# Kernel optimization log

Hardware: AMD Instinct MI355X
Metric: run time of the kernel (lower is better)

The kernel has to match this reference:

```python
import jax, jax.numpy as jnp
import numpy as np

B, Hd, Wd, C, NH, WS = 8, 128, 128, 192, 6, 8
HDIM = int(C * 2.0)   # FFN hidden = 384
RED = C // 8          # AIM channel-gate reduction = 24


def setup_inputs() -> dict:
    key = jax.random.key(0)
    ks = jax.random.split(key, 12)
    s = 0.02
    return {
        "x": jax.random.normal(ks[0], (B, Hd * Wd, C), jnp.float32),
        "H": Hd,
        "W": Wd,
        "n1_w": jnp.ones((C,), jnp.float32),
        "n1_b": jnp.zeros((C,), jnp.float32),
        "qkv_w": jax.random.normal(ks[1], (C, 3 * C), jnp.float32) * s,
        "proj_w": jax.random.normal(ks[2], (C, C), jnp.float32) * s,
        "proj_b": jnp.zeros((C,), jnp.float32),
        "attn_bias": jax.random.normal(ks[3], (NH, WS * WS, WS * WS), jnp.float32) * s,
        "conv_w": jax.random.normal(ks[4], (C, 1, 3, 3), jnp.float32) * s,
        "cg_w1": jax.random.normal(ks[5], (RED, C), jnp.float32) * s,
        "cg_w2": jax.random.normal(ks[6], (C, RED), jnp.float32) * s,
        "n2_w": jnp.ones((C,), jnp.float32),
        "n2_b": jnp.zeros((C,), jnp.float32),
        "fc1_w": jax.random.normal(ks[7], (C, HDIM), jnp.float32) * s,
        "smix_w": jax.random.normal(ks[8], (HDIM, 1, 3, 3), jnp.float32) * s,
        "fc2_w": jax.random.normal(ks[9], (HDIM, C), jnp.float32) * s,
    }


def _ln(x, w, b):
    m = x.mean(-1, keepdims=True)
    v = ((x - m) ** 2).mean(-1, keepdims=True)
    return (x - m) * jax.lax.rsqrt(v + 1e-5) * w + b


def _dwconv(x, w, H, W):
    # x: [B, L, Cx] -> depthwise 3x3 'same' conv -> [B, L, Cx]
    Bx, L, Cx = x.shape
    xi = x.transpose(0, 2, 1).reshape(Bx, Cx, H, W)
    y = jax.lax.conv_general_dilated(
        xi, w, (1, 1), 'SAME', feature_group_count=Cx,
        dimension_numbers=('NCHW', 'OIHW', 'NCHW'))
    return y.reshape(Bx, Cx, L).transpose(0, 2, 1)


def _window_attn(x, H, W, qkv_w, proj_w, proj_b, bias):
    Bx, L, Cx = x.shape
    nHw, nWw = H // WS, W // WS  # H, W are multiples of WS here (no padding needed)
    hd = Cx // NH
    # [B, L, C] -> [B*nH*nW, ws*ws, C]
    xw = (x.reshape(Bx, nHw, WS, nWw, WS, Cx)
           .transpose(0, 1, 3, 2, 4, 5)
           .reshape(Bx * nHw * nWw, WS * WS, Cx))
    qkv = (xw @ qkv_w).reshape(-1, WS * WS, 3, NH, hd).transpose(2, 0, 3, 1, 4)
    q, k, v = qkv[0], qkv[1], qkv[2]          # [Bw, nh, N, hd]
    logits = (q * hd ** -0.5) @ k.transpose(0, 1, 3, 2) + bias[None]
    attn = jax.nn.softmax(logits, axis=-1)
    out = (attn @ v).transpose(0, 2, 1, 3).reshape(-1, WS * WS, Cx)
    out = out @ proj_w + proj_b
    # windows -> [B, L, C]
    return (out.reshape(Bx, nHw, nWw, WS, WS, Cx)
               .transpose(0, 1, 3, 2, 4, 5)
               .reshape(Bx, L, Cx))


def reference(x, H, W, n1_w, n1_b, qkv_w, proj_w, proj_b, attn_bias,
              conv_w, cg_w1, cg_w2, n2_w, n2_b, fc1_w, smix_w, fc2_w):
    n1 = _ln(x, n1_w, n1_b)
    attn_feat = _window_attn(n1, H, W, qkv_w, proj_w, proj_b, attn_bias)
    conv_feat = jax.nn.gelu(_dwconv(n1, conv_w, H, W), approximate=False)
    # AIM: channel_modulates_spatial (btype == 'spatial')
    pooled = conv_feat.mean(axis=1)                                   # [B, C]
    cm = jax.nn.sigmoid(jax.nn.gelu(pooled @ cg_w1.T, approximate=False) @ cg_w2.T)
    x = x + attn_feat * cm[:, None, :] + conv_feat                    # residual (DropPath=id)
    # FFN with depthwise spatial mixing
    n2 = _ln(x, n2_w, n2_b)
    h = jax.nn.gelu(n2 @ fc1_w, approximate=False)                    # [B, L, HDIM]
    h = _dwconv(h, smix_w, H, W)
    return x + h @ fc2_w
```

## Files before the change

kernel.cpp:

```cpp
#include <hip/hip_runtime.h>
#include <hip/hip_bf16.h>
#include <math.h>

#define BATCH 8
#define CCH 192
#define LTOK 16384
#define BL 131072LL
#define NWIN 2048
#define NHEADS 6

typedef __hip_bfloat16 bf16;
typedef __bf16 bfr;
typedef bfr bf16x8 __attribute__((ext_vector_type(8)));
typedef float f32x4 __attribute__((ext_vector_type(4)));
typedef unsigned short u16x8 __attribute__((ext_vector_type(8)));
typedef unsigned short u16x4 __attribute__((ext_vector_type(4)));
typedef unsigned int u32x2 __attribute__((ext_vector_type(2)));

#define FX     0
#define FN1W   1
#define FN1B   2
#define FQKVW  3
#define FPROJW 4
#define FPROJB 5
#define FBIAS  6
#define FCONVW 7
#define FCG1   8
#define FCG2   9
#define FN2W   10
#define FN2B   11
#define FFC1   12
#define FSMIX  13
#define FFC2   14

struct InPtrs { const void* p[15]; int n[15]; };

__device__ __forceinline__ float ldin(const void* p, long long i, int f32) {
    return f32 ? ((const float*)p)[i]
               : __bfloat162float(((const bf16*)p)[i]);
}

__device__ __forceinline__ float bfcvt(unsigned short u) {
    return __uint_as_float((unsigned)u << 16);
}

__device__ __forceinline__ f32x4 ld4f(const void* p, long long i, int f32) {
    if (f32) return *(const f32x4*)((const float*)p + i);
    u16x4 v = *(const u16x4*)((const bf16*)p + i);
    f32x4 r;
    r[0] = bfcvt(v[0]); r[1] = bfcvt(v[1]); r[2] = bfcvt(v[2]); r[3] = bfcvt(v[3]);
    return r;
}
__device__ __forceinline__ f32x4 ld4b(const bf16* p, long long i) {
    u16x4 v = *(const u16x4*)(p + i);
    f32x4 r;
    r[0] = bfcvt(v[0]); r[1] = bfcvt(v[1]); r[2] = bfcvt(v[2]); r[3] = bfcvt(v[3]);
    return r;
}
__device__ __forceinline__ void st4b(bf16* p, long long i, f32x4 v) {
    union { bf16 h; unsigned short u; } cv;
    u16x4 o;
    cv.h = __float2bfloat16(v[0]); o[0] = cv.u;
    cv.h = __float2bfloat16(v[1]); o[1] = cv.u;
    cv.h = __float2bfloat16(v[2]); o[2] = cv.u;
    cv.h = __float2bfloat16(v[3]); o[3] = cv.u;
    *(u16x4*)(p + i) = o;
}

__device__ __forceinline__ unsigned pk2bf(float a, float b) {
    union { bf16 h; unsigned short u; } ca, cb;
    ca.h = __float2bfloat16(a);
    cb.h = __float2bfloat16(b);
    return (unsigned)ca.u | ((unsigned)cb.u << 16);
}

__device__ __forceinline__ float gelu_f(float v) {
    return 0.5f * v * (1.0f + erff(v * 0.70710678118654752f));
}

__device__ int local_probe(const void* p_, int n) {
    __shared__ int sh0, sh1, sh2;
    if (threadIdx.x == 0) { sh0 = 0; sh1 = 0; sh2 = 0; }
    __syncthreads();
    const bf16* p = (const bf16*)p_;
    int m = n < 2048 ? n : 2048;
    bool insane = false, evennz = false, oddnz = false;
    for (int i = threadIdx.x; i < m; i += 256) {
        float v = __bfloat162float(p[i]);
        if (!(fabsf(v) <= 1e9f)) insane = true;
        if (v != 0.0f) { if (i & 1) oddnz = true; else evennz = true; }
    }
    if (insane) sh0 = 1;
    if (evennz) sh1 = 1;
    if (oddnz)  sh2 = 1;
    __syncthreads();
    return (sh0 || (!sh1 && sh2)) ? 1 : 0;
}

__global__ __launch_bounds__(256)
void prep_k(InPtrs ip, int* __restrict__ flags,
            bf16* __restrict__ qkv_wT, bf16* __restrict__ proj_wT,
            bf16* __restrict__ fc1_wT, bf16* __restrict__ fc2_wT,
            float* __restrict__ convwT, float* __restrict__ smixwT,
            float* __restrict__ pooled) {
    int blk = blockIdx.x;
    if (blk < 15) {
        int f = local_probe(ip.p[blk], ip.n[blk]);
        if (threadIdx.x == 0) flags[blk] = f;
        return;
    }
    blk -= 15;
    if (blk < 432) {
        int f = local_probe(ip.p[FQKVW], ip.n[FQKVW]);
        int idx = blk * 256 + threadIdx.x;
        int k = idx / 576, n = idx - k * 576;
        qkv_wT[(long long)n * 192 + k] = __float2bfloat16(ldin(ip.p[FQKVW], idx, f));
        return;
    }
    blk -= 432;
    if (blk < 144) {
        int f = local_probe(ip.p[FPROJW], ip.n[FPROJW]);
        int idx = blk * 256 + threadIdx.x;
        int k = idx / 192, n = idx - k * 192;
        proj_wT[(long long)n * 192 + k] = __float2bfloat16(ldin(ip.p[FPROJW], idx, f));
        return;
    }
    blk -= 144;
    if (blk < 288) {
        int f = local_probe(ip.p[FFC1], ip.n[FFC1]);
        int idx = blk * 256 + threadIdx.x;
        int k = idx / 384, n = idx - k * 384;
        fc1_wT[(long long)n * 192 + k] = __float2bfloat16(ldin(ip.p[FFC1], idx, f));
        return;
    }
    blk -= 288;
    if (blk < 288) {
        int f = local_probe(ip.p[FFC2], ip.n[FFC2]);
        int idx = blk * 256 + threadIdx.x;
        int k = idx / 192, n = idx - k * 192;
        fc2_wT[(long long)n * 384 + k] = __float2bfloat16(ldin(ip.p[FFC2], idx, f));
        return;
    }
    blk -= 288;
    if (blk < 7) {
        int f = local_probe(ip.p[FCONVW], ip.n[FCONVW]);
        int idx = blk * 256 + threadIdx.x;
        if (idx < 192 * 9) {
            int c = idx / 9, t = idx - c * 9;
            convwT[t * 192 + c] = ldin(ip.p[FCONVW], idx, f);
        }
        return;
    }
    blk -= 7;
    if (blk < 14) {
        int f = local_probe(ip.p[FSMIX], ip.n[FSMIX]);
        int idx = blk * 256 + threadIdx.x;
        if (idx < 384 * 9) {
            int c = idx / 9, t = idx - c * 9;
            smixwT[t * 384 + c] = ldin(ip.p[FSMIX], idx, f);
        }
        return;
    }
    blk -= 14;
    {
        int idx = blk * 256 + threadIdx.x;
        if (idx < BATCH * CCH) pooled[idx] = 0.f;
    }
}

__global__ __launch_bounds__(256)
void ln_kernel(const void* __restrict__ x, const void* __restrict__ w,
               const void* __restrict__ b, bf16* __restrict__ out,
               const int* flags) {
    int fx = flags[FX], fw = flags[FN1W], fb = flags[FN1B];
    int wv = threadIdx.x >> 6, lane = threadIdx.x & 63;
    int gw = lane >> 4, l16 = lane & 15;
    long long t = (long long)blockIdx.x * 16 + wv * 4 + gw;
    long long base = t * CCH;
    f32x4 v[3];
#pragma unroll
    for (int k = 0; k < 3; ++k)
        v[k] = ld4f(x, base + l16 * 4 + 64 * k, fx);
    float s = 0.f;
#pragma unroll
    for (int k = 0; k < 3; ++k) s += v[k][0] + v[k][1] + v[k][2] + v[k][3];
    s += __shfl_xor(s, 1); s += __shfl_xor(s, 2);
    s += __shfl_xor(s, 4); s += __shfl_xor(s, 8);
    float mean = s * (1.0f / 192.0f);
    float vs = 0.f;
#pragma unroll
    for (int k = 0; k < 3; ++k)
#pragma unroll
        for (int j = 0; j < 4; ++j) {
            float d = v[k][j] - mean;
            vs += d * d;
        }
    vs += __shfl_xor(vs, 1); vs += __shfl_xor(vs, 2);
    vs += __shfl_xor(vs, 4); vs += __shfl_xor(vs, 8);
    float rstd = rsqrtf(vs * (1.0f / 192.0f) + 1e-5f);
#pragma unroll
    for (int k = 0; k < 3; ++k) {
        int c0 = l16 * 4 + 64 * k;
        f32x4 wv4 = ld4f(w, c0, fw);
        f32x4 bv4 = ld4f(b, c0, fb);
        f32x4 o;
#pragma unroll
        for (int j = 0; j < 4; ++j)
            o[j] = (v[k][j] - mean) * rstd * wv4[j] + bv4[j];
        st4b(out, base + c0, o);
    }
}

template<int EPI, int KK, int NN, typename CT>
__global__ __launch_bounds__(256)
void gemm2_k(const bf16* __restrict__ A_, const bf16* __restrict__ BT_,
             CT* __restrict__ Cmat, const void* __restrict__ bias,
             const float* __restrict__ res, const int* __restrict__ flags) {
    constexpr int KT = KK / 192;
    constexpr int NC = NN / 64;
    constexpr int NITER = NC * KT;
    constexpr int GSTR = KK * 2;
    constexpr bool WINM = (EPI == 0);
    __shared__ __align__(16) char Ts[64 * 384];

    const int fb = (EPI == 1) ? flags[FPROJB] : 0;
    const int tid = threadIdx.x;
    const int lane = tid & 63, wv = tid >> 6;
    const int r16 = lane & 15, q = lane >> 4;
    const long long m0 = (long long)blockIdx.x * 64;
    const int swz = (r16 & 7) << 4;

    const int wdx = blockIdx.x;
    const int wb = wdx >> 8, wrem = wdx & 255, wy = wrem >> 4, wx = wrem & 15;
    const long long tokbase = (long long)wb * LTOK + (wy * 8) * 128 + wx * 8;

    f32x4 pre[6];
    auto loadB = [&](int itn) {
        int nc2 = itn / KT, kt2 = itn - nc2 * KT;
#pragma unroll
        for (int p = 0; p < 6; ++p) {
            int off = p * 4096 + tid * 16;
            int row = off / 384, col = off - row * 384;
            pre[p] = *(const f32x4*)((const char*)BT_ +
                     (long long)(nc2 * 64 + row) * GSTR + kt2 * 384 + col);
        }
    };
    auto writeT = [&]() {
#pragma unroll
        for (int p = 0; p < 6; ++p) {
            int off = p * 4096 + tid * 16;
            int row = off / 384, col = off - row * 384;
            *(f32x4*)(Ts + row * 384 + (col ^ ((row & 7) << 4))) = pre[p];
        }
    };

    loadB(0);

    bf16x8 afrag[KK / 32];
    const char* Arow = Ts + (wv * 16 + r16) * 384;
    const char* asrc = (const char*)A_;
#pragma unroll
    for (int kt = 0; kt < KT; ++kt) {
#pragma unroll
        for (int p = 0; p < 6; ++p) {
            int off = p * 4096 + tid * 16;
            int row = off / 384, col = off - row * 384;
            long long grow = WINM ? (tokbase + (row >> 3) * 128 + (row & 7))
                                  : (m0 + row);
            *(f32x4*)(Ts + row * 384 + (col ^ ((row & 7) << 4))) =
                *(const f32x4*)(asrc + grow * GSTR + kt * 384 + col);
        }
        __syncthreads();
#pragma unroll
        for (int ks = 0; ks < 6; ++ks)
            afrag[kt * 6 + ks] = *(const bf16x8*)(Arow + ((ks * 64 + q * 16) ^ swz));
        __syncthreads();
    }
    writeT();
    __syncthreads();

    f32x4 acc0, acc1, acc2, acc3;
    float resv[16];

    for (int it = 0; it < NITER; ++it) {
        const int nc = it / KT, kt = it - nc * KT;
        if (kt == 0) {
            acc0 = f32x4{0.f, 0.f, 0.f, 0.f};
            acc1 = acc0; acc2 = acc0; acc3 = acc0;
            if (EPI == 3) {
#pragma unroll
                for (int j = 0; j < 4; ++j)
#pragma unroll
                    for (int r = 0; r < 4; ++r)
                        resv[j * 4 + r] =
                            res[(m0 + wv * 16 + q * 4 + r) * NN + nc * 64 + j * 16 + r16];
            }
        }
        const bool nxt = (it + 1 < NITER);
        if (nxt) loadB(it + 1);
#pragma unroll
        for (int ks = 0; ks < 6; ++ks) {
            bf16x8 a = afrag[kt * 6 + ks];
            const char* bb = Ts + r16 * 384 + ((ks * 64 + q * 16) ^ swz);
            bf16x8 b0 = *(const bf16x8*)(bb);
            bf16x8 b1 = *(const bf16x8*)(bb + 16 * 384);
            bf16x8 b2 = *(const bf16x8*)(bb + 32 * 384);
            bf16x8 b3 = *(const bf16x8*)(bb + 48 * 384);
            acc0 = __builtin_amdgcn_mfma_f32_16x16x32_bf16(a, b0, acc0, 0, 0, 0);
            acc1 = __builtin_amdgcn_mfma_f32_16x16x32_bf16(a, b1, acc1, 0, 0, 0);
            acc2 = __builtin_amdgcn_mfma_f32_16x16x32_bf16(a, b2, acc2, 0, 0, 0);
            acc3 = __builtin_amdgcn_mfma_f32_16x16x32_bf16(a, b3, acc3, 0, 0, 0);
        }
        __syncthreads();
        if (nxt) writeT();
        if (kt == KT - 1) {
            f32x4 accs[4] = {acc0, acc1, acc2, acc3};
#pragma unroll
            for (int j = 0; j < 4; ++j) {
                int col = nc * 64 + j * 16 + r16;
#pragma unroll
                for (int r = 0; r < 4; ++r) {
                    float v = accs[j][r];
                    if (EPI == 1) v += ldin(bias, col, fb);
                    if (EPI == 2) v = gelu_f(v);
                    if (EPI == 3) v += resv[j * 4 + r];
                    if (WINM) {
                        int tin = wv * 16 + q * 4 + r;
                        int sel = col / 192, rem2 = col - sel * 192;
                        int hh = rem2 >> 5, d = rem2 & 31;
                        Cmat[((((long long)sel * NWIN + wdx) * 6 + hh) * 64 + tin) * 32 + d] = (CT)v;
                    } else {
                        long long row = m0 + wv * 16 + q * 4 + r;
                        Cmat[row * NN + col] = (CT)v;
                    }
                }
            }
        }
        if (nxt) __syncthreads();
    }
}

__global__ __launch_bounds__(768)
void attn_proj_k(const bf16* __restrict__ qkvw, const void* __restrict__ bias,
                 const bf16* __restrict__ pwT, const void* __restrict__ proj_b,
                 bf16* __restrict__ attnf, const int* __restrict__ flags) {
    __shared__ __align__(16) char SM[24576];

    const int fbias = flags[FBIAS];
    const int wid = threadIdx.x >> 6, lane = threadIdx.x & 63;
    const int h = wid >> 1, half = wid & 1;
    const int w = blockIdx.x;
    const int l15 = lane & 15, quad = lane >> 4;
    bfr* vtp = (bfr*)(SM + h * 4096);

    const bfr* qb = (const bfr*)qkvw + ((long long)w * 6 + h) * 2048;
    const bfr* kb = qb + (long long)NWIN * 6 * 2048;
    const bfr* vb = kb + (long long)NWIN * 6 * 2048;

    if (half == 0) {
        const bfr* vp = vb + lane * 32;
        bf16x8 v0 = *(const bf16x8*)(vp);
        bf16x8 v1 = *(const bf16x8*)(vp + 8);
        bf16x8 v2 = *(const bf16x8*)(vp + 16);
        bf16x8 v3 = *(const bf16x8*)(vp + 24);
#pragma unroll
        for (int j = 0; j < 8; ++j) {
            int sc = lane ^ (j << 3);
            vtp[j * 64 + sc]        = v0[j];
            vtp[(j + 8) * 64 + sc]  = v1[j];
            vtp[(j + 16) * 64 + sc] = v2[j];
            vtp[(j + 24) * 64 + sc] = v3[j];
        }
    }

    bf16x8 bk[4], aq[2];
#pragma unroll
    for (int ti = 0; ti < 4; ++ti)
        bk[ti] = *(const bf16x8*)(kb + (ti * 16 + l15) * 32 + quad * 8);
#pragma unroll
    for (int tj2 = 0; tj2 < 2; ++tj2)
        aq[tj2] = *(const bf16x8*)(qb + ((half * 2 + tj2) * 16 + l15) * 32 + quad * 8);

    const float scale = 0.17677669529663689f;
    const long long bias0 = (long long)h * 4096;
    unsigned Wreg[2][4][2];
#pragma unroll
    for (int tj2 = 0; tj2 < 2; ++tj2) {
        const int tj = half * 2 + tj2;
        f32x4 T[4];
#pragma unroll
        for (int ti = 0; ti < 4; ++ti) {
            f32x4 z = {0.f, 0.f, 0.f, 0.f};
            T[ti] = __builtin_amdgcn_mfma_f32_16x16x32_bf16(bk[ti], aq[tj2], z, 0, 0, 0);
        }
        const long long brow = bias0 + (tj * 16 + l15) * 64 + quad * 4;
        float mloc = -3.0e38f;
#pragma unroll
        for (int ti = 0; ti < 4; ++ti) {
            f32x4 bv4 = ld4f(bias, brow + ti * 16, fbias);
#pragma unroll
            for (int r = 0; r < 4; ++r) {
                float v = T[ti][r] * scale + bv4[r];
                T[ti][r] = v;
                mloc = fmaxf(mloc, v);
            }
        }
        mloc = fmaxf(mloc, __shfl_xor(mloc, 16));
        mloc = fmaxf(mloc, __shfl_xor(mloc, 32));
        float l = 0.f;
#pragma unroll
        for (int ti = 0; ti < 4; ++ti)
#pragma unroll
            for (int r = 0; r < 4; ++r) {
                float e = __expf(T[ti][r] - mloc);
                T[ti][r] = e;
                l += e;
            }
        l += __shfl_xor(l, 16);
        l += __shfl_xor(l, 32);
        float linv = 1.0f / l;
#pragma unroll
        for (int ti = 0; ti < 4; ++ti) {
            Wreg[tj2][ti][0] = pk2bf(T[ti][0] * linv, T[ti][1] * linv);
            Wreg[tj2][ti][1] = pk2bf(T[ti][2] * linv, T[ti][3] * linv);
        }
    }

    __syncthreads();

    const int vsw = (l15 & 7) << 3;
    bf16x8 bv[2][2];
#pragma unroll
    for (int kc = 0; kc < 2; ++kc) {
        bv[kc][0] = *(const bf16x8*)&vtp[l15 * 64 + ((kc * 32 + quad * 8) ^ vsw)];
        bv[kc][1] = *(const bf16x8*)&vtp[(16 + l15) * 64 + ((kc * 32 + quad * 8) ^ vsw)];
    }
    const int hi = quad >> 1, qlow = quad & 1;
    f32x4 O[2][2];
#pragma unroll
    for (int tj2 = 0; tj2 < 2; ++tj2) {
        O[tj2][0] = f32x4{0.f, 0.f, 0.f, 0.f};
        O[tj2][1] = O[tj2][0];
    }
#pragma unroll
    for (int tj2 = 0; tj2 < 2; ++tj2)
#pragma unroll
        for (int kc = 0; kc < 2; ++kc) {
            union { unsigned u[4]; bf16x8 v; } ap;
#pragma unroll
            for (int j2 = 0; j2 < 4; ++j2) {
                int srcl = (2 * qlow + (j2 >> 1)) * 16 + l15;
                unsigned va = (unsigned)__shfl((int)Wreg[tj2][2 * kc][j2 & 1], srcl);
                unsigned vb2 = (unsigned)__shfl((int)Wreg[tj2][2 * kc + 1][j2 & 1], srcl);
                ap.u[j2] = hi ? vb2 : va;
            }
            O[tj2][0] = __builtin_amdgcn_mfma_f32_16x16x32_bf16(ap.v, bv[kc][0], O[tj2][0], 0, 0, 0);
            O[tj2][1] = __builtin_amdgcn_mfma_f32_16x16x32_bf16(ap.v, bv[kc][1], O[tj2][1], 0, 0, 0);
        }

    const int fpb = flags[FPROJB];
    const int pcol = wid * 16 + l15;
    float pbv = ldin(proj_b, pcol, fpb);
    bf16x8 pw[6];
#pragma unroll
    for (int ks = 0; ks < 6; ++ks)
        pw[ks] = *(const bf16x8*)((const bfr*)pwT + (long long)pcol * 192 + ks * 32 + quad * 8);

    __syncthreads();

#pragma unroll
    for (int tj2 = 0; tj2 < 2; ++tj2)
#pragma unroll
        for (int n2 = 0; n2 < 2; ++n2)
#pragma unroll
            for (int r = 0; r < 4; ++r) {
                int row = (half * 2 + tj2) * 16 + quad * 4 + r;
                int cb = (h * 64 + n2 * 32 + l15 * 2) ^ ((row & 7) << 4);
                *(bf16*)(SM + row * 384 + cb) = __float2bfloat16(O[tj2][n2][r]);
            }

    __syncthreads();

    const int csw = (l15 & 7) << 4;
    f32x4 pacc[4];
#pragma unroll
    for (int mt = 0; mt < 4; ++mt)
        pacc[mt] = f32x4{0.f, 0.f, 0.f, 0.f};
#pragma unroll
    for (int ks = 0; ks < 6; ++ks) {
#pragma unroll
        for (int mt = 0; mt < 4; ++mt) {
            bf16x8 af = *(const bf16x8*)(SM + (mt * 16 + l15) * 384 +
                                         ((ks * 64 + quad * 16) ^ csw));
            pacc[mt] = __builtin_amdgcn_mfma_f32_16x16x32_bf16(af, pw[ks], pacc[mt], 0, 0, 0);
        }
    }

#pragma unroll
    for (int mt = 0; mt < 4; ++mt)
#pragma unroll
        for (int r = 0; r < 4; ++r) {
            long long row = (long long)w * 64 + mt * 16 + quad * 4 + r;
            attnf[row * CCH + pcol] = __float2bfloat16(pacc[mt][r] + pbv);
        }
}

template<bool GELU, int CX, bool POOL>
__global__ __launch_bounds__(256)
void dwconv_s4_k(const bf16* __restrict__ in, const float* __restrict__ wt,
                 bf16* __restrict__ out, float* __restrict__ pooled) {
    constexpr int CG = CX / 8;
    __shared__ float psum[POOL ? 192 : 1];
    if (POOL) {
        if (threadIdx.x < 192) psum[threadIdx.x] = 0.f;
        __syncthreads();
    }
    int cpx = gridDim.x >> 3;
    int lb = (blockIdx.x & 7) * cpx + (blockIdx.x >> 3);
    long long idx = (long long)lb * 256 + threadIdx.x;
    int cg = (int)(idx % CG);
    long long s = idx / CG;
    int xs = (int)(s & 31);
    long long by = s >> 5;
    int y = (int)(by & 127);
    int x0 = xs * 4;
    int c0 = cg * 8;
    const long long rowpix = by * 128;

    float acc[4][8] = {};
#pragma unroll
    for (int dy = -1; dy <= 1; ++dy) {
        int yy = y + dy;
        if (yy < 0 || yy > 127) continue;
        const bf16* rp = in + ((rowpix + dy * 128) + x0) * CX + c0;
        float fcol[6][8];
#pragma unroll
        for (int ci = 0; ci < 6; ++ci) {
            int xx = x0 + ci - 1;
            if (xx < 0 || xx > 127) {
#pragma unroll
                for (int j = 0; j < 8; ++j) fcol[ci][j] = 0.f;
            } else {
                u16x8 v = *(const u16x8*)(rp + (ci - 1) * CX);
#pragma unroll
                for (int j = 0; j < 8; ++j) fcol[ci][j] = bfcvt(v[j]);
            }
        }
        const float* wb = wt + (dy + 1) * 3 * CX + c0;
#pragma unroll
        for (int dx = 0; dx < 3; ++dx) {
            f32x4 w0 = *(const f32x4*)(wb + dx * CX);
            f32x4 w1 = *(const f32x4*)(wb + dx * CX + 4);
#pragma unroll
            for (int px = 0; px < 4; ++px) {
#pragma unroll
                for (int j = 0; j < 4; ++j) {
                    acc[px][j]     += fcol[px + dx][j]     * w0[j];
                    acc[px][j + 4] += fcol[px + dx][j + 4] * w1[j];
                }
            }
        }
    }
    float sums[8] = {0.f, 0.f, 0.f, 0.f, 0.f, 0.f, 0.f, 0.f};
#pragma unroll
    for (int px = 0; px < 4; ++px) {
        __attribute__((aligned(16))) unsigned short ob[8];
#pragma unroll
        for (int j = 0; j < 8; ++j) {
            float vv = acc[px][j];
            if (GELU) vv = gelu_f(vv);
            if (POOL) sums[j] += vv;
            union { bf16 h; unsigned short u; } cv;
            cv.h = __float2bfloat16(vv);
            ob[j] = cv.u;
        }
        *(u16x8*)(out + (rowpix + x0 + px) * CX + c0) = *(const u16x8*)ob;
    }
    if (POOL) {
#pragma unroll
        for (int j = 0; j < 8; ++j)
            atomicAdd(&psum[c0 + j], sums[j]);
        __syncthreads();
        if (threadIdx.x < 192) {
            int b = (int)(by >> 7);
            atomicAdd(&pooled[b * CCH + threadIdx.x], psum[threadIdx.x]);
        }
    }
}

__global__ void cm_k(const float* __restrict__ pooled, const void* __restrict__ w1,
                     const void* __restrict__ w2, float* __restrict__ cm,
                     const int* flags) {
    __shared__ float ps[192], g[24];
    int f1 = flags[FCG1], f2 = flags[FCG2];
    int b = blockIdx.x, c = threadIdx.x;
    ps[c] = pooled[b * CCH + c] * (1.0f / 16384.0f);
    __syncthreads();
    if (c < 24) {
        float t = 0.f;
        for (int k = 0; k < 192; ++k) t += ps[k] * ldin(w1, c * 192 + k, f1);
        g[c] = gelu_f(t);
    }
    __syncthreads();
    float s = 0.f;
#pragma unroll
    for (int r = 0; r < 24; ++r) s += g[r] * ldin(w2, c * 24 + r, f2);
    cm[b * CCH + c] = 1.0f / (1.0f + expf(-s));
}

__global__ __launch_bounds__(256)
void x2ln2_k(const void* __restrict__ x, const bf16* __restrict__ attnf,
             const bf16* __restrict__ conv, const float* __restrict__ cm,
             const void* __restrict__ w, const void* __restrict__ bb,
             float* __restrict__ x2, bf16* __restrict__ n2, const int* flags) {
    int fx = flags[FX], fw = flags[FN2W], fb = flags[FN2B];
    int wv = threadIdx.x >> 6, lane = threadIdx.x & 63;
    int gw = lane >> 4, l16 = lane & 15;
    long long t = (long long)blockIdx.x * 16 + wv * 4 + gw;
    int b = (int)(t >> 14);
    int l = (int)(t & 16383);
    int y = l >> 7, xx = l & 127;
    long long wrow = ((long long)b * 256 + (y >> 3) * 16 + (xx >> 3)) * 64 + (y & 7) * 8 + (xx & 7);

    f32x4 sv[3];
#pragma unroll
    for (int k = 0; k < 3; ++k) {
        int c0 = l16 * 4 + 64 * k;
        f32x4 xv  = ld4f(x, t * CCH + c0, fx);
        f32x4 af  = ld4b(attnf, wrow * CCH + c0);
        f32x4 cf  = ld4b(conv, t * CCH + c0);
        f32x4 cmv = *(const f32x4*)(cm + b * CCH + c0);
        f32x4 o;
#pragma unroll
        for (int j = 0; j < 4; ++j)
            o[j] = xv[j] + af[j] * cmv[j] + cf[j];
        *(f32x4*)(x2 + t * CCH + c0) = o;
        sv[k] = o;
    }
    float s = 0.f;
#pragma unroll
    for (int k = 0; k < 3; ++k) s += sv[k][0] + sv[k][1] + sv[k][2] + sv[k][3];
    s += __shfl_xor(s, 1); s += __shfl_xor(s, 2);
    s += __shfl_xor(s, 4); s += __shfl_xor(s, 8);
    float mean = s * (1.0f / 192.0f);
    float vs = 0.f;
#pragma unroll
    for (int k = 0; k < 3; ++k)
#pragma unroll
        for (int j = 0; j < 4; ++j) {
            float d = sv[k][j] - mean;
            vs += d * d;
        }
    vs += __shfl_xor(vs, 1); vs += __shfl_xor(vs, 2);
    vs += __shfl_xor(vs, 4); vs += __shfl_xor(vs, 8);
    float rstd = rsqrtf(vs * (1.0f / 192.0f) + 1e-5f);
#pragma unroll
    for (int k = 0; k < 3; ++k) {
        int c0 = l16 * 4 + 64 * k;
        f32x4 wv4 = ld4f(w, c0, fw);
        f32x4 bv4 = ld4f(bb, c0, fb);
        f32x4 o;
#pragma unroll
        for (int j = 0; j < 4; ++j)
            o[j] = (sv[k][j] - mean) * rstd * wv4[j] + bv4[j];
        st4b(n2, t * CCH + c0, o);
    }
}

extern "C" void kernel_launch(void* const* d_in, const int* in_sizes, int n_in,
                              void* d_out, int out_size, void* d_ws, size_t ws_size,
                              hipStream_t stream) {
    (void)n_in; (void)out_size; (void)ws_size;
    float* out = (float*)d_out;

    char* wsp = (char*)d_ws;
    size_t off = 0;
    auto alloc = [&](size_t bytes) -> char* {
        char* p = wsp + off;
        off += (bytes + 255) & ~(size_t)255;
        return p;
    };
    int*  flags   = (int*)alloc(15 * 4);
    bf16* qkv_wT  = (bf16*)alloc(576 * 192 * 2);
    bf16* proj_wT = (bf16*)alloc(192 * 192 * 2);
    bf16* fc1_wT  = (bf16*)alloc(384 * 192 * 2);
    bf16* fc2_wT  = (bf16*)alloc(192 * 384 * 2);
    float* convwT = (float*)alloc(9 * CCH * 4);
    float* smixwT = (float*)alloc(9 * 384 * 4);
    float* pooled = (float*)alloc(BATCH * CCH * 4);
    float* cm     = (float*)alloc(BATCH * CCH * 4);
    char* Rbig    = alloc(BL * 576 * 2);
    char* Rpair   = alloc(BL * 384 * 2);

    bf16* qkvb  = (bf16*)Rbig;
    bf16* convf = (bf16*)Rbig;
    bf16* hbuf  = (bf16*)Rbig;
    bf16* n1    = (bf16*)Rpair;
    bf16* attnf = (bf16*)(Rpair + (size_t)BL * 192 * 2);
    bf16* n2    = n1;
    bf16* h2    = (bf16*)Rpair;
    float* x2   = out;

    const int imap[15] = {0, 3, 4, 5, 6, 7, 8, 9, 10, 11, 12, 13, 14, 15, 16};
    InPtrs ip;
    for (int i = 0; i < 15; ++i) { ip.p[i] = d_in[imap[i]]; ip.n[i] = in_sizes[imap[i]]; }
    const void* x        = d_in[0];
    const void* proj_b   = d_in[7];
    const void* attnbias = d_in[8];
    const void* cg_w1    = d_in[10];
    const void* cg_w2    = d_in[11];

    prep_k<<<1194, 256, 0, stream>>>(ip, flags, qkv_wT, proj_wT, fc1_wT, fc2_wT,
                                     convwT, smixwT, pooled);

    ln_kernel<<<BL / 16, 256, 0, stream>>>(x, d_in[3], d_in[4], n1, flags);
    gemm2_k<0, 192, 576, bf16><<<BL / 64, 256, 0, stream>>>(n1, qkv_wT, qkvb, nullptr, nullptr, flags);
    attn_proj_k<<<NWIN, 768, 0, stream>>>(qkvb, attnbias, proj_wT, proj_b, attnf, flags);
    dwconv_s4_k<true, 192, true><<<(int)(BL / 4 * 24 / 256), 256, 0, stream>>>(n1, convwT, convf, pooled);
    cm_k<<<BATCH, 192, 0, stream>>>(pooled, cg_w1, cg_w2, cm, flags);
    x2ln2_k<<<BL / 16, 256, 0, stream>>>(x, attnf, convf, cm, d_in[12], d_in[13], x2, n2, flags);
    gemm2_k<2, 192, 384, bf16><<<BL / 64, 256, 0, stream>>>(n2, fc1_wT, hbuf, nullptr, nullptr, flags);
    dwconv_s4_k<false, 384, false><<<(int)(BL / 4 * 48 / 256), 256, 0, stream>>>(hbuf, smixwT, h2, nullptr);
    gemm2_k<3, 384, 192, float><<<BL / 64, 256, 0, stream>>>(h2, fc2_wT, out, nullptr, x2, flags);
}
```

Before: 592.6 us.

## Merge window attention and depthwise conv into one heterogeneous launch

Combines the attention+projection kernel and the GELU depthwise conv + pooling kernel into one grid. The first NWIN blocks do attention and the extra blocks do conv with 768 threads each. This removes a launch boundary and lets the memory-bound conv overlap the MFMA-heavy attention. Because conv output previously aliased the qkv buffer, it now goes to a separate workspace buffer. The merged path is used only when the workspace is large enough, otherwise it falls back to the two separate kernels. Costs are extra workspace and a different block shape for the conv (768 threads, 1024 blocks).

```diff
diff --git a/kernel.cpp b/kernel.cpp
--- a/kernel.cpp
+++ b/kernel.cpp
@@ -340,16 +340,14 @@
     }
 }
 
-__global__ __launch_bounds__(768)
-void attn_proj_k(const bf16* __restrict__ qkvw, const void* __restrict__ bias,
-                 const bf16* __restrict__ pwT, const void* __restrict__ proj_b,
-                 bf16* __restrict__ attnf, const int* __restrict__ flags) {
-    __shared__ __align__(16) char SM[24576];
-
+__device__ __forceinline__
+void attn_body(int w, char* SM, const bf16* __restrict__ qkvw,
+               const void* __restrict__ bias, const bf16* __restrict__ pwT,
+               const void* __restrict__ proj_b, bf16* __restrict__ attnf,
+               const int* __restrict__ flags) {
     const int fbias = flags[FBIAS];
     const int wid = threadIdx.x >> 6, lane = threadIdx.x & 63;
     const int h = wid >> 1, half = wid & 1;
-    const int w = blockIdx.x;
     const int l15 = lane & 15, quad = lane >> 4;
     bfr* vtp = (bfr*)(SM + h * 4096);
 
@@ -505,19 +503,16 @@
         }
 }
 
-template<bool GELU, int CX, bool POOL>
-__global__ __launch_bounds__(256)
-void dwconv_s4_k(const bf16* __restrict__ in, const float* __restrict__ wt,
-                 bf16* __restrict__ out, float* __restrict__ pooled) {
+template<bool GELU, int CX, bool POOL, int TPB>
+__device__ __forceinline__
+void dwconv_body(int lb, const bf16* __restrict__ in, const float* __restrict__ wt,
+                 bf16* __restrict__ out, float* __restrict__ pooled, float* psum) {
     constexpr int CG = CX / 8;
-    __shared__ float psum[POOL ? 192 : 1];
     if (POOL) {
         if (threadIdx.x < 192) psum[threadIdx.x] = 0.f;
         __syncthreads();
     }
-    int cpx = gridDim.x >> 3;
-    int lb = (blockIdx.x & 7) * cpx + (blockIdx.x >> 3);
-    long long idx = (long long)lb * 256 + threadIdx.x;
+    long long idx = (long long)lb * TPB + threadIdx.x;
     int cg = (int)(idx % CG);
     long long s = idx / CG;
     int xs = (int)(s & 31);
@@ -586,6 +581,40 @@
             atomicAdd(&pooled[b * CCH + threadIdx.x], psum[threadIdx.x]);
         }
     }
+}
+
+__global__ __launch_bounds__(768)
+void attn_conv_k(const bf16* __restrict__ qkvw, const void* __restrict__ bias,
+                 const bf16* __restrict__ pwT, const void* __restrict__ proj_b,
+                 bf16* __restrict__ attnf, const int* __restrict__ flags,
+                 const bf16* __restrict__ n1, const float* __restrict__ convwT,
+                 bf16* __restrict__ convf, float* __restrict__ pooled) {
+    __shared__ __align__(16) char SM[24576];
+    if (blockIdx.x >= NWIN) {
+        int dblk = blockIdx.x - NWIN;
+        int lb = (dblk & 7) * 128 + (dblk >> 3);
+        dwconv_body<true, 192, true, 768>(lb, n1, convwT, convf, pooled, (float*)SM);
+        return;
+    }
+    attn_body(blockIdx.x, SM, qkvw, bias, pwT, proj_b, attnf, flags);
+}
+
+__global__ __launch_bounds__(768)
+void attn_proj_k(const bf16* __restrict__ qkvw, const void* __restrict__ bias,
+                 const bf16* __restrict__ pwT, const void* __restrict__ proj_b,
+                 bf16* __restrict__ attnf, const int* __restrict__ flags) {
+    __shared__ __align__(16) char SM[24576];
+    attn_body(blockIdx.x, SM, qkvw, bias, pwT, proj_b, attnf, flags);
+}
+
+template<bool GELU, int CX, bool POOL>
+__global__ __launch_bounds__(256)
+void dwconv_s4_k(const bf16* __restrict__ in, const float* __restrict__ wt,
+                 bf16* __restrict__ out, float* __restrict__ pooled) {
+    __shared__ float psum[POOL ? 192 : 1];
+    int cpx = gridDim.x >> 3;
+    int lb = (blockIdx.x & 7) * cpx + (blockIdx.x >> 3);
+    dwconv_body<GELU, CX, POOL, 256>(lb, in, wt, out, pooled, psum);
 }
 
 __global__ void cm_k(const float* __restrict__ pooled, const void* __restrict__ w1,
@@ -670,7 +699,7 @@
 extern "C" void kernel_launch(void* const* d_in, const int* in_sizes, int n_in,
                               void* d_out, int out_size, void* d_ws, size_t ws_size,
                               hipStream_t stream) {
-    (void)n_in; (void)out_size; (void)ws_size;
+    (void)n_in; (void)out_size;
     float* out = (float*)d_out;
 
     char* wsp = (char*)d_ws;
@@ -691,9 +720,11 @@
     float* cm     = (float*)alloc(BATCH * CCH * 4);
     char* Rbig    = alloc(BL * 576 * 2);
     char* Rpair   = alloc(BL * 384 * 2);
+    bf16* convf2  = (bf16*)alloc((size_t)BL * 192 * 2);
+    const bool merged = (ws_size >= off);
 
     bf16* qkvb  = (bf16*)Rbig;
-    bf16* convf = (bf16*)Rbig;
+    bf16* convf = merged ? convf2 : (bf16*)Rbig;
     bf16* hbuf  = (bf16*)Rbig;
     bf16* n1    = (bf16*)Rpair;
     bf16* attnf = (bf16*)(Rpair + (size_t)BL * 192 * 2);
@@ -715,8 +746,13 @@
 
     ln_kernel<<<BL / 16, 256, 0, stream>>>(x, d_in[3], d_in[4], n1, flags);
     gemm2_k<0, 192, 576, bf16><<<BL / 64, 256, 0, stream>>>(n1, qkv_wT, qkvb, nullptr, nullptr, flags);
-    attn_proj_k<<<NWIN, 768, 0, stream>>>(qkvb, attnbias, proj_wT, proj_b, attnf, flags);
-    dwconv_s4_k<true, 192, true><<<(int)(BL / 4 * 24 / 256), 256, 0, stream>>>(n1, convwT, convf, pooled);
+    if (merged) {
+        attn_conv_k<<<NWIN + 1024, 768, 0, stream>>>(qkvb, attnbias, proj_wT, proj_b,
+                                                     attnf, flags, n1, convwT, convf, pooled);
+    } else {
+        attn_proj_k<<<NWIN, 768, 0, stream>>>(qkvb, attnbias, proj_wT, proj_b, attnf, flags);
+        dwconv_s4_k<true, 192, true><<<(int)(BL / 4 * 24 / 256), 256, 0, stream>>>(n1, convwT, convf, pooled);
+    }
     cm_k<<<BATCH, 192, 0, stream>>>(pooled, cg_w1, cg_w2, cm, flags);
     x2ln2_k<<<BL / 16, 256, 0, stream>>>(x, attnf, convf, cm, d_in[12], d_in[13], x2, n2, flags);
     gemm2_k<2, 192, 384, bf16><<<BL / 64, 256, 0, stream>>>(n2, fc1_wT, hbuf, nullptr, nullptr, flags);
```

Measured after the change: 606.9 us. 1.02x slower.

## Fuse FFN depthwise conv into fc2 GEMM A-tile load

Applied to the files above, without the earlier changes.

Removes the separate depthwise 3x3 spatial-mix kernel on the FFN hidden activations. The fc2 GEMM now computes the 3x3 depthwise conv on the fly while staging each 64-token A tile into shared memory. This drops a full write and read of the 384-channel intermediate buffer. In exchange, each GEMM block reads up to 9 neighbouring token vectors per element and does the conv arithmetic inside the GEMM, which adds load traffic and register pressure to the GEMM prologue.

```diff
diff --git a/kernel.cpp b/kernel.cpp
--- a/kernel.cpp
+++ b/kernel.cpp
@@ -211,11 +211,12 @@
     }
 }
 
-template<int EPI, int KK, int NN, typename CT>
+template<int EPI, int KK, int NN, typename CT, bool CONVA = false>
 __global__ __launch_bounds__(256)
 void gemm2_k(const bf16* __restrict__ A_, const bf16* __restrict__ BT_,
              CT* __restrict__ Cmat, const void* __restrict__ bias,
-             const float* __restrict__ res, const int* __restrict__ flags) {
+             const float* __restrict__ res, const int* __restrict__ flags,
+             const float* __restrict__ cwt = nullptr) {
     constexpr int KT = KK / 192;
     constexpr int NC = NN / 64;
     constexpr int NITER = NC * KT;
@@ -234,6 +235,10 @@
     const int wb = wdx >> 8, wrem = wdx & 255, wy = wrem >> 4, wx = wrem & 15;
     const long long tokbase = (long long)wb * LTOK + (wy * 8) * 128 + wx * 8;
 
+    const int l0 = (int)(m0 & 16383);
+    const int yy0 = l0 >> 7, xx0 = l0 & 127;
+    const long long imgbase = m0 - l0;
+
     f32x4 pre[6];
     auto loadB = [&](int itn) {
         int nc2 = itn / KT, kt2 = itn - nc2 * KT;
@@ -265,10 +270,44 @@
         for (int p = 0; p < 6; ++p) {
             int off = p * 4096 + tid * 16;
             int row = off / 384, col = off - row * 384;
-            long long grow = WINM ? (tokbase + (row >> 3) * 128 + (row & 7))
-                                  : (m0 + row);
-            *(f32x4*)(Ts + row * 384 + (col ^ ((row & 7) << 4))) =
-                *(const f32x4*)(asrc + grow * GSTR + kt * 384 + col);
+            if (CONVA) {
+                int c0 = kt * 192 + (col >> 1);
+                int px = xx0 + row;
+                float acc[8] = {};
+#pragma unroll
+                for (int dy = -1; dy <= 1; ++dy) {
+                    int yv = yy0 + dy;
+                    if (yv < 0 || yv > 127) continue;
+#pragma unroll
+                    for (int dx = -1; dx <= 1; ++dx) {
+                        int xv = px + dx;
+                        if (xv < 0 || xv > 127) continue;
+                        u16x8 hv = *(const u16x8*)((const bf16*)A_ +
+                                   (imgbase + yv * 128 + xv) * KK + c0);
+                        const float* wr = cwt + ((dy + 1) * 3 + (dx + 1)) * KK + c0;
+                        f32x4 w0 = *(const f32x4*)(wr);
+                        f32x4 w1 = *(const f32x4*)(wr + 4);
+#pragma unroll
+                        for (int j = 0; j < 4; ++j) {
+                            acc[j]     += bfcvt(hv[j])     * w0[j];
+                            acc[j + 4] += bfcvt(hv[j + 4]) * w1[j];
+                        }
+                    }
+                }
+                union { u16x8 v; unsigned short u[8]; } ob;
+#pragma unroll
+                for (int j = 0; j < 8; ++j) {
+                    union { bf16 h; unsigned short u; } cv;
+                    cv.h = __float2bfloat16(acc[j]);
+                    ob.u[j] = cv.u;
+                }
+                *(u16x8*)(Ts + row * 384 + (col ^ ((row & 7) << 4))) = ob.v;
+            } else {
+                long long grow = WINM ? (tokbase + (row >> 3) * 128 + (row & 7))
+                                      : (m0 + row);
+                *(f32x4*)(Ts + row * 384 + (col ^ ((row & 7) << 4))) =
+                    *(const f32x4*)(asrc + grow * GSTR + kt * 384 + col);
+            }
         }
         __syncthreads();
 #pragma unroll
@@ -698,7 +737,6 @@
     bf16* n1    = (bf16*)Rpair;
     bf16* attnf = (bf16*)(Rpair + (size_t)BL * 192 * 2);
     bf16* n2    = n1;
-    bf16* h2    = (bf16*)Rpair;
     float* x2   = out;
 
     const int imap[15] = {0, 3, 4, 5, 6, 7, 8, 9, 10, 11, 12, 13, 14, 15, 16};
@@ -720,6 +758,5 @@
     cm_k<<<BATCH, 192, 0, stream>>>(pooled, cg_w1, cg_w2, cm, flags);
     x2ln2_k<<<BL / 16, 256, 0, stream>>>(x, attnf, convf, cm, d_in[12], d_in[13], x2, n2, flags);
     gemm2_k<2, 192, 384, bf16><<<BL / 64, 256, 0, stream>>>(n2, fc1_wT, hbuf, nullptr, nullptr, flags);
-    dwconv_s4_k<false, 384, false><<<(int)(BL / 4 * 48 / 256), 256, 0, stream>>>(hbuf, smixwT, h2, nullptr);
-    gemm2_k<3, 384, 192, float><<<BL / 64, 256, 0, stream>>>(h2, fc2_wT, out, nullptr, x2, flags);
-}
+    gemm2_k<3, 384, 192, float, true><<<BL / 64, 256, 0, stream>>>(hbuf, fc2_wT, out, nullptr, x2, flags, smixwT);
+}
```

New measurement: 685.2 us. 1.16x slower.
